# Performance work log

Measured on AMD Instinct MI355X. Metric: run time of the kernel, lower is better.

The kernel has to match this reference:

```python
import jax, jax.numpy as jnp
import numpy as np

B, S, D = 4, 2048, 1024
N_HEAD = 16
D_HEAD = D // N_HEAD
WINDOW = 1024
D_FF = 4 * D
EPS = 1e-5
NEG = -1e10


def _layernorm(x, g, b):
    mu = jnp.mean(x, axis=-1, keepdims=True)
    var = jnp.mean(jnp.square(x - mu), axis=-1, keepdims=True)
    return (x - mu) * jax.lax.rsqrt(var + EPS) * g + b


def setup_inputs() -> dict:
    key = jax.random.key(0)
    ks = jax.random.split(key, 12)
    s = 1.0 / np.sqrt(D)
    x = jax.random.normal(ks[0], (B, S, D), dtype=jnp.float32)
    key_pad_mask = jax.random.bernoulli(ks[1], 0.1, (B, S))
    return {
        "x": x,
        "key_pad_mask": key_pad_mask,
        "ln1_g": jnp.ones((D,), jnp.float32),
        "ln1_b": jnp.zeros((D,), jnp.float32),
        "wq": jax.random.normal(ks[2], (D, D), jnp.float32) * s,
        "bq": jnp.zeros((D,), jnp.float32),
        "wkv": jax.random.normal(ks[3], (D, 2 * D), jnp.float32) * s,
        "bkv": jnp.zeros((2 * D,), jnp.float32),
        "ln2_g": jnp.ones((D,), jnp.float32),
        "ln2_b": jnp.zeros((D,), jnp.float32),
        "w1": jax.random.normal(ks[4], (D, D_FF), jnp.float32) * s,
        "b1": jnp.zeros((D_FF,), jnp.float32),
        "w2": jax.random.normal(ks[5], (D_FF, D), jnp.float32) * (1.0 / np.sqrt(D_FF)),
        "b2": jnp.zeros((D,), jnp.float32),
    }


def reference(x, key_pad_mask, ln1_g, ln1_b, wq, bq, wkv, bkv, ln2_g, ln2_b, w1, b1, w2, b2):
    ln1x = _layernorm(x, ln1_g, ln1_b)
    # queries over full sequence: [B, S, nh, dh]
    q = (ln1x @ wq + bq).reshape(B, S, N_HEAD, D_HEAD)
    # keys/values from the last WINDOW tokens: [B, W, 2*nh, dh]
    kv = (ln1x[:, -WINDOW:, :] @ wkv + bkv).reshape(B, WINDOW, 2 * N_HEAD, D_HEAD)
    k, v = kv[..., :N_HEAD, :], kv[..., N_HEAD:, :]
    # NOTE: original scales by sqrt(embed_dim), not sqrt(head_dim)
    scores = jnp.einsum('bqhd,bkhd->bhqk', q, k) / np.sqrt(D)
    causal = jnp.triu(jnp.ones((S, WINDOW), dtype=bool), k=1)  # faithful to original
    pad = key_pad_mask[:, None, None, -WINDOW:]
    scores = jnp.where(pad | causal[None, None], jnp.float32(NEG), scores)
    attn = jax.nn.softmax(scores, axis=-1)
    out = jnp.einsum('bhqk,bkhd->bqhd', attn, v).reshape(B, S, D)
    h = _layernorm(out, ln2_g, ln2_b)
    h = jax.nn.silu(h @ w1 + b1) @ w2 + b2
    return h + x
```

## Files before the change

kernel.cpp:

```cpp
#include <hip/hip_runtime.h>
#include <hip/hip_bf16.h>

#define BB 4
#define SS 2048
#define DD 1024
#define HH 16
#define DHH 64
#define WW 1024
#define DFF 4096
#define MM (BB*SS)
#define NEGV (-1e10f)
#define KSC 0.045084220027780106f

using f32x4 = __attribute__((ext_vector_type(4))) float;
using s16x8 = __attribute__((ext_vector_type(8))) short;
using s16x4 = __attribute__((ext_vector_type(4))) short;
using u64 = unsigned long long;

typedef const __attribute__((address_space(1))) void* gas_t;
typedef __attribute__((address_space(3))) void* las_t;

__device__ inline short f2b(float f) {
  __hip_bfloat16 h = __float2bfloat16(f);
  return __builtin_bit_cast(short, h);
}
__device__ inline float b2f(short u) {
  __hip_bfloat16 h = __builtin_bit_cast(__hip_bfloat16, u);
  return __bfloat162float(h);
}

__device__ inline void gload_lds16(const short* g, short* lds) {
  __builtin_amdgcn_global_load_lds((gas_t)g, (las_t)lds, 16, 0, 0);
}

__device__ inline f32x4 mfma16(s16x8 a, s16x8 b, f32x4 c) {
  return __builtin_amdgcn_mfma_f32_16x16x32_bf16(a, b, c, 0, 0, 0);
}

template<int IN_BF16>
__global__ __launch_bounds__(256) void ln_kernel(const void* __restrict__ inp,
                                                 const float* __restrict__ g,
                                                 const float* __restrict__ bta,
                                                 short* __restrict__ outp) {
  int row = blockIdx.x;
  int t = threadIdx.x;
  float v[4];
  if constexpr (IN_BF16) {
    s16x4 r4 = *((const s16x4*)((const short*)inp + (size_t)row*DD) + t);
    v[0]=b2f(r4[0]); v[1]=b2f(r4[1]); v[2]=b2f(r4[2]); v[3]=b2f(r4[3]);
  } else {
    f32x4 r4 = *((const f32x4*)((const float*)inp + (size_t)row*DD) + t);
    v[0]=r4[0]; v[1]=r4[1]; v[2]=r4[2]; v[3]=r4[3];
  }
  float s = v[0]+v[1]+v[2]+v[3];
  float sq = v[0]*v[0]+v[1]*v[1]+v[2]*v[2]+v[3]*v[3];
  for (int m=1;m<64;m<<=1){ s += __shfl_xor(s,m); sq += __shfl_xor(sq,m); }
  __shared__ float red[8];
  int wv = t>>6;
  if ((t&63)==0){ red[wv]=s; red[4+wv]=sq; }
  __syncthreads();
  s  = red[0]+red[1]+red[2]+red[3];
  sq = red[4]+red[5]+red[6]+red[7];
  float mean = s*(1.f/DD);
  float rstd = rsqrtf(sq*(1.f/DD) - mean*mean + 1e-5f);
  int col = t*4;
  s16x4 o;
  #pragma unroll
  for (int j=0;j<4;++j) o[j] = f2b((v[j]-mean)*rstd*g[col+j]+bta[col+j]);
  *((s16x4*)(outp + (size_t)row*DD) + t) = o;
}

__global__ __launch_bounds__(256) void transpose_cast(const float* __restrict__ in,
                                                      short* __restrict__ out,
                                                      int K, int N) {
  __shared__ float tile[32][33];
  int n0 = blockIdx.x*32, k0 = blockIdx.y*32;
  int tx = threadIdx.x & 31, ty = threadIdx.x >> 5;
  #pragma unroll
  for (int j=0;j<4;++j) tile[ty+8*j][tx] = in[(size_t)(k0+ty+8*j)*N + n0+tx];
  __syncthreads();
  #pragma unroll
  for (int j=0;j<4;++j) out[(size_t)(n0+ty+8*j)*K + k0+tx] = f2b(tile[tx][ty+8*j]);
}

__global__ void pad_bitmask(const int* __restrict__ pad, u64* __restrict__ pm) {
  int idx = threadIdx.x;
  int b_ = idx>>4, col = idx&15;
  const int* pb = pad + b_*SS + (SS-WW);
  u64 m = 0;
  for (int c=0;c<16;++c)
    for (int nf=0;nf<4;++nf)
      if (pb[c*64+nf*16+col]) m |= (1ull << (c*4+nf));
  pm[idx] = m;
}

template<int EPI>
__global__ __launch_bounds__(512) void gemm256(const short* __restrict__ A,
                                               const short* __restrict__ Bt,
                                               const float* __restrict__ bias,
                                               void* __restrict__ out1,
                                               int N, int K, int lgx) {
  __shared__ short lds[32768];
  int tid = threadIdx.x, l = tid&63, wid = tid>>6;
  int wm = wid>>2, wn = wid&3;
  int q8 = gridDim.x >> 3;
  int wg = (blockIdx.x & 7)*q8 + (blockIdx.x >> 3);
  int bx = wg & ((1<<lgx)-1), by = wg >> lgx;
  const short* Ablk = A + (size_t)by*256*K;
  const short* Bblk = Bt + (size_t)bx*256*K;
  int rA = l & 15;
  int slot_s = ((l>>4) ^ ((rA>>1)&3))*8;
  int aBase = (wm*128 + rA)*32 + slot_s;
  int bBase = (wn*64  + rA)*32 + slot_s + 8192;
  int qs = (tid&3) ^ ((tid>>3)&3);
  const short* srcA = Ablk + (size_t)(tid>>2)*K + qs*8;
  const short* srcB = Bblk + (size_t)(tid>>2)*K + qs*8;
  int dst0 = (tid & ~63)*8;
  int nt = K >> 5;
  f32x4 acc[8][4];
  #pragma unroll
  for (int i=0;i<8;++i)
    #pragma unroll
    for (int j=0;j<4;++j)
      #pragma unroll
      for (int r=0;r<4;++r) acc[i][j][r]=0.f;

  auto stage = [&](int isB, int b, int t) {
    const short* s = isB ? srcB : srcA;
    short* d = &lds[b*16384 + isB*8192 + dst0];
    gload_lds16(s + t*32,                 d);
    gload_lds16(s + (size_t)128*K + t*32, d + 4096);
  };
  s16x8 af[4], bf[4];
  auto readA = [&](int b, int mg) {
    #pragma unroll
    for (int j=0;j<4;++j) af[j] = *(const s16x8*)&lds[b*16384 + aBase + (mg*4+j)*512];
  };
  auto readB = [&](int b) {
    #pragma unroll
    for (int j=0;j<4;++j) bf[j] = *(const s16x8*)&lds[b*16384 + bBase + j*512];
  };
  auto mfmas = [&](int mg) {
    __builtin_amdgcn_s_setprio(1);
    #pragma unroll
    for (int j=0;j<4;++j)
      #pragma unroll
      for (int nf=0;nf<4;++nf)
        acc[mg*4+j][nf] = mfma16(af[j], bf[nf], acc[mg*4+j][nf]);
    __builtin_amdgcn_s_setprio(0);
  };

  stage(0,0,0); stage(1,0,0); stage(1,1,1);
  asm volatile("s_waitcnt vmcnt(2)" ::: "memory");
  __builtin_amdgcn_s_barrier();

  for (int it = 0; it < (nt>>1); ++it) {
    int t0 = 2*it;
    int t2 = t0+2; if (t2 >= nt) t2 -= nt;
    int t3 = t0+3; if (t3 >= nt) t3 -= nt;
    readB(0); readA(0,0);
    stage(0,1,t0+1);
    __builtin_amdgcn_s_barrier();
    mfmas(0);
    __builtin_amdgcn_s_barrier();
    readA(0,1);
    stage(1,0,t2);
    __builtin_amdgcn_s_barrier();
    mfmas(1);
    asm volatile("s_waitcnt vmcnt(2)" ::: "memory");
    __builtin_amdgcn_s_barrier();
    readB(1); readA(1,0);
    stage(0,0,t2);
    __builtin_amdgcn_s_barrier();
    mfmas(0);
    __builtin_amdgcn_s_barrier();
    readA(1,1);
    stage(1,1,t3);
    __builtin_amdgcn_s_barrier();
    mfmas(1);
    asm volatile("s_waitcnt vmcnt(2)" ::: "memory");
    __builtin_amdgcn_s_barrier();
  }
  asm volatile("s_waitcnt vmcnt(0)" ::: "memory");

  #pragma unroll
  for (int mf=0;mf<8;++mf) {
    #pragma unroll
    for (int nf=0;nf<4;++nf) {
      #pragma unroll
      for (int r=0;r<4;++r) {
        int row = by*256 + wm*128 + mf*16 + ((l>>4)<<2) + r;
        int col = bx*256 + wn*64 + nf*16 + rA;
        float v = acc[mf][nf][r] + bias[col];
        if constexpr (EPI==2) {
          float sv = v / (1.f + __expf(-v));
          ((short*)out1)[(size_t)row*N + col] = f2b(sv);
        } else {
          ((short*)out1)[(size_t)row*N + col] = f2b(v);
        }
      }
    }
  }
}

template<int EPI>
__global__ __launch_bounds__(512) void gemm256x128(const short* __restrict__ A,
                                                   const short* __restrict__ Bt,
                                                   const float* __restrict__ bias,
                                                   void* __restrict__ out1,
                                                   void* __restrict__ out2,
                                                   const float* __restrict__ resid,
                                                   int N, int K, int lgx) {
  __shared__ short lds[24576];
  int tid = threadIdx.x, l = tid&63, wid = tid>>6;
  int wm = wid>>1, wn = wid&1;
  int q8 = gridDim.x >> 3;
  int wg = (blockIdx.x & 7)*q8 + (blockIdx.x >> 3);
  int bx = wg & ((1<<lgx)-1), by = wg >> lgx;
  const short* Ablk;
  if constexpr (EPI==1) {
    int b_ = (by*256)>>10, w0 = (by*256)&1023;
    Ablk = A + ((size_t)b_*SS + (SS-WW) + w0)*DD;
  } else {
    Ablk = A + (size_t)by*256*K;
  }
  const short* Bblk = Bt + (size_t)bx*128*K;
  int rA = l & 15;
  int slot_s = ((l>>4) ^ ((rA>>1)&3))*8;
  int aBase = (wm*64 + rA)*32 + slot_s;
  int bBase = 8192 + (wn*64 + rA)*32 + slot_s;
  int qs = (tid&3) ^ ((tid>>3)&3);
  const short* srcA = Ablk + (size_t)(tid>>2)*K + qs*8;
  const short* srcB = Bblk + (size_t)(tid>>2)*K + qs*8;
  int dst0 = (tid & ~63)*8;
  int nt = K >> 5;
  f32x4 acc[4][4];
  #pragma unroll
  for (int i=0;i<4;++i)
    #pragma unroll
    for (int j=0;j<4;++j)
      #pragma unroll
      for (int r=0;r<4;++r) acc[i][j][r]=0.f;

  auto stageA = [&](int b, int t) {
    short* d = &lds[b*12288 + dst0];
    gload_lds16(srcA + t*32,                 d);
    gload_lds16(srcA + (size_t)128*K + t*32, d + 4096);
  };
  auto stageB = [&](int b, int t) {
    gload_lds16(srcB + t*32, &lds[b*12288 + 8192 + dst0]);
  };
  s16x8 af[2], bf[4];
  auto readA = [&](int b, int mg) {
    #pragma unroll
    for (int j=0;j<2;++j) af[j] = *(const s16x8*)&lds[b*12288 + aBase + (mg*2+j)*512];
  };
  auto readB = [&](int b) {
    #pragma unroll
    for (int j=0;j<4;++j) bf[j] = *(const s16x8*)&lds[b*12288 + bBase + j*512];
  };
  auto mfmas = [&](int mg) {
    __builtin_amdgcn_s_setprio(1);
    #pragma unroll
    for (int j=0;j<2;++j)
      #pragma unroll
      for (int nf=0;nf<4;++nf)
        acc[mg*2+j][nf] = mfma16(af[j], bf[nf], acc[mg*2+j][nf]);
    __builtin_amdgcn_s_setprio(0);
  };

  stageA(0,0); stageB(0,0); stageB(1,1);
  asm volatile("s_waitcnt vmcnt(1)" ::: "memory");
  __builtin_amdgcn_s_barrier();

  for (int it = 0; it < (nt>>1); ++it) {
    int t0 = 2*it;
    int t2 = t0+2; if (t2 >= nt) t2 -= nt;
    int t3 = t0+3; if (t3 >= nt) t3 -= nt;
    readB(0); readA(0,0);
    stageA(1,t0+1);
    __builtin_amdgcn_s_barrier();
    mfmas(0);
    __builtin_amdgcn_s_barrier();
    readA(0,1);
    stageB(0,t2);
    __builtin_amdgcn_s_barrier();
    mfmas(1);
    asm volatile("s_waitcnt vmcnt(1)" ::: "memory");
    __builtin_amdgcn_s_barrier();
    readB(1); readA(1,0);
    stageA(0,t2);
    __builtin_amdgcn_s_barrier();
    mfmas(0);
    __builtin_amdgcn_s_barrier();
    readA(1,1);
    stageB(1,t3);
    __builtin_amdgcn_s_barrier();
    mfmas(1);
    asm volatile("s_waitcnt vmcnt(1)" ::: "memory");
    __builtin_amdgcn_s_barrier();
  }
  asm volatile("s_waitcnt vmcnt(0)" ::: "memory");

  #pragma unroll
  for (int mf=0;mf<4;++mf) {
    #pragma unroll
    for (int nf=0;nf<4;++nf) {
      #pragma unroll
      for (int r=0;r<4;++r) {
        int row = by*256 + wm*64 + mf*16 + ((l>>4)<<2) + r;
        int col = bx*128 + wn*64 + nf*16 + rA;
        float v = acc[mf][nf][r] + bias[col];
        if constexpr (EPI==0) {
          ((short*)out1)[(size_t)row*N + col] = f2b(v);
        } else if constexpr (EPI==1) {
          int b_ = row>>10, w_ = row&1023;
          if (col < DD) {
            int h = col>>6, dh = col&63;
            ((short*)out1)[(((size_t)(b_*HH+h))*WW + w_)*DHH + dh] = f2b(v*KSC);
          } else {
            int cc = col - DD;
            int h = cc>>6, dh = cc&63;
            ((short*)out2)[(((size_t)(b_*HH+h))*DHH + dh)*WW + w_] = f2b(v);
          }
        } else {
          ((float*)out1)[(size_t)row*N + col] = v + resid[(size_t)row*N + col];
        }
      }
    }
  }
}

struct KF { s16x8 v[4][2]; };

__global__ __launch_bounds__(64,2) void attn_kernel(const short* __restrict__ q,
    const short* __restrict__ kpan, const short* __restrict__ vtpan,
    const u64* __restrict__ pmarr, short* __restrict__ outp) {
  __shared__ short P[32*72];
  int l = threadIdx.x;
  int id = blockIdx.x;
  int xcd = id & 7, slot = id >> 3;
  int bh = xcd + 8*(slot >> 6);
  int u  = 63 - (slot & 63);
  int bb = bh >> 4, h = bh & 15;
  int r0 = u*32;
  const short* kbase = kpan + (size_t)bh*WW*DHH;
  const short* vbase = vtpan + (size_t)bh*DHH*WW;
  u64 pmask = pmarr[bb*16 + (l&15)];
  const s16x8 ones8 = { 0x3F80,0x3F80,0x3F80,0x3F80,0x3F80,0x3F80,0x3F80,0x3F80 };

  s16x8 aq[2][2];
  #pragma unroll
  for (int g=0;g<2;++g)
    #pragma unroll
    for (int kf=0;kf<2;++kf)
      aq[g][kf] = *(const s16x8*)(q + ((size_t)bb*SS + r0 + g*16 + (l&15))*DD
                                    + h*DHH + (l>>4)*8 + kf*32);
  f32x4 oacc[2][4];
  float mrun[2][4], lrun[2][4], scale[2][4];
  #pragma unroll
  for (int g=0;g<2;++g)
    #pragma unroll
    for (int i=0;i<4;++i) {
      #pragma unroll
      for (int r=0;r<4;++r) oacc[g][i][r]=0.f;
      mrun[g][i]=-INFINITY; lrun[g][i]=0.f;
    }
  int dchunk = u>>1;
  int nch = dchunk+1 < 16 ? dchunk+1 : 16;

  auto loadK = [&](int c, KF& d) {
    const short* kc = kbase + (size_t)c*64*DHH;
    #pragma unroll
    for (int nf=0;nf<4;++nf) {
      const short* p = kc + (size_t)(nf*16+(l&15))*DHH + ((l>>4)*8);
      d.v[nf][0] = *(const s16x8*)p;
      d.v[nf][1] = *(const s16x8*)(p+32);
    }
  };

  auto body = [&](int c, KF& kf) {
    f32x4 sc[2][4];
    #pragma unroll
    for (int g=0;g<2;++g)
      #pragma unroll
      for (int nf=0;nf<4;++nf)
        #pragma unroll
        for (int r=0;r<4;++r) sc[g][nf][r]=0.f;
    __builtin_amdgcn_s_setprio(1);
    #pragma unroll
    for (int nf=0;nf<4;++nf)
      #pragma unroll
      for (int g=0;g<2;++g) {
        sc[g][nf] = mfma16(aq[g][0], kf.v[nf][0], sc[g][nf]);
        sc[g][nf] = mfma16(aq[g][1], kf.v[nf][1], sc[g][nf]);
      }
    __builtin_amdgcn_s_setprio(0);
    unsigned nib = (unsigned)(pmask >> (c*4)) & 15u;
    float pm[2][4];
    #pragma unroll
    for (int g=0;g<2;++g)
      #pragma unroll
      for (int r=0;r<4;++r) pm[g][r] = -INFINITY;
    if (c >= dchunk) {
      #pragma unroll
      for (int nf=0;nf<4;++nf) {
        int j = c*64 + nf*16 + (l&15);
        int padj = (int)((nib>>nf)&1u);
        #pragma unroll
        for (int g=0;g<2;++g)
          #pragma unroll
          for (int r=0;r<4;++r) {
            int sq_ = r0 + g*16 + ((l>>4)<<2) + r;
            float xv = (padj || (j > sq_)) ? NEGV : sc[g][nf][r];
            sc[g][nf][r] = xv;
            pm[g][r] = fmaxf(pm[g][r], xv);
          }
      }
    } else {
      #pragma unroll
      for (int nf=0;nf<4;++nf) {
        int padj = (int)((nib>>nf)&1u);
        #pragma unroll
        for (int g=0;g<2;++g)
          #pragma unroll
          for (int r=0;r<4;++r) {
            float xv = padj ? NEGV : sc[g][nf][r];
            sc[g][nf][r] = xv;
            pm[g][r] = fmaxf(pm[g][r], xv);
          }
      }
    }
    s16x8 vf0[4], vf1[4];
    #pragma unroll
    for (int nf=0;nf<4;++nf)
      vf0[nf] = *(const s16x8*)(vbase + (size_t)(nf*16+(l&15))*WW
                                + c*64 + ((l>>4)*8));
    int need = 0;
    #pragma unroll
    for (int g=0;g<2;++g)
      #pragma unroll
      for (int r=0;r<4;++r) need |= (pm[g][r] > mrun[g][r] + 12.f) ? 1 : 0;
    #pragma unroll
    for (int g=0;g<2;++g)
      #pragma unroll
      for (int r=0;r<4;++r) scale[g][r] = 1.f;
    if (__any(need)) {
      #pragma unroll
      for (int m=1;m<16;m<<=1)
        #pragma unroll
        for (int g=0;g<2;++g)
          #pragma unroll
          for (int r=0;r<4;++r) pm[g][r] = fmaxf(pm[g][r], __shfl_xor(pm[g][r], m));
      #pragma unroll
      for (int g=0;g<2;++g)
        #pragma unroll
        for (int r=0;r<4;++r) {
          float mn = fmaxf(mrun[g][r], pm[g][r]);
          scale[g][r] = exp2f(mrun[g][r]-mn);
          mrun[g][r] = mn;
        }
      #pragma unroll
      for (int g=0;g<2;++g)
        #pragma unroll
        for (int nf=0;nf<4;++nf)
          #pragma unroll
          for (int r=0;r<4;++r) oacc[g][nf][r] *= scale[g][r];
    }
    #pragma unroll
    for (int nf=0;nf<4;++nf)
      #pragma unroll
      for (int g=0;g<2;++g)
        #pragma unroll
        for (int r=0;r<4;++r)
          sc[g][nf][r] = exp2f(sc[g][nf][r]-mrun[g][r]);
    #pragma unroll
    for (int nf=0;nf<4;++nf)
      vf1[nf] = *(const s16x8*)(vbase + (size_t)(nf*16+(l&15))*WW
                                + c*64 + 32 + ((l>>4)*8));
    #pragma unroll
    for (int g=0;g<2;++g)
      #pragma unroll
      for (int nf=0;nf<4;++nf)
        #pragma unroll
        for (int r=0;r<4;++r)
          P[(g*16+((l>>4)<<2)+r)*72 + nf*16 + (l&15)] = f2b(sc[g][nf][r]);
    f32x4 ls2[2];
    #pragma unroll
    for (int g=0;g<2;++g)
      #pragma unroll
      for (int r=0;r<4;++r) ls2[g][r]=0.f;
    __builtin_amdgcn_s_setprio(1);
    #pragma unroll
    for (int ks=0;ks<2;++ks) {
      s16x8 ap[2];
      #pragma unroll
      for (int g=0;g<2;++g) {
        ap[g] = *(const s16x8*)&P[(g*16+(l&15))*72 + ks*32 + ((l>>4)*8)];
        ls2[g] = mfma16(ap[g], ones8, ls2[g]);
      }
      #pragma unroll
      for (int nf=0;nf<4;++nf) {
        s16x8 bv = ks ? vf1[nf] : vf0[nf];
        #pragma unroll
        for (int g=0;g<2;++g)
          oacc[g][nf] = mfma16(ap[g], bv, oacc[g][nf]);
      }
    }
    __builtin_amdgcn_s_setprio(0);
    #pragma unroll
    for (int g=0;g<2;++g)
      #pragma unroll
      for (int r=0;r<4;++r) lrun[g][r] = lrun[g][r]*scale[g][r] + ls2[g][r];
  };

  KF ka, kb;
  loadK(0, ka);
  int cend = nch, c = 0, ext = 0;
  while (true) {
    if (c == cend) {
      if (ext) break;
      ext = 1;
      int dead = 0;
      #pragma unroll
      for (int g=0;g<2;++g)
        #pragma unroll
        for (int r=0;r<4;++r) dead |= (mrun[g][r] < -5e9f) ? 1 : 0;
      if (!__any(dead)) break;
      cend = 16;
      if (c >= 16) break;
    }
    if (c+1 < 16) loadK(c+1, kb);
    body(c, ka);
    ka = kb;
    ++c;
  }

  #pragma unroll
  for (int g=0;g<2;++g)
    #pragma unroll
    for (int nf=0;nf<4;++nf)
      #pragma unroll
      for (int r=0;r<4;++r) {
        int srow = r0 + g*16 + ((l>>4)<<2) + r;
        float o = oacc[g][nf][r] / lrun[g][r];
        outp[((size_t)bb*SS + srow)*DD + h*DHH + nf*16 + (l&15)] = f2b(o);
      }
}

extern "C" void kernel_launch(void* const* d_in, const int* in_sizes, int n_in,
                              void* d_out, int out_size, void* d_ws, size_t ws_size,
                              hipStream_t stream) {
  const float* x    = (const float*)d_in[0];
  const int*   pad  = (const int*)d_in[1];
  const float* ln1g = (const float*)d_in[2];
  const float* ln1b = (const float*)d_in[3];
  const float* wq   = (const float*)d_in[4];
  const float* bq   = (const float*)d_in[5];
  const float* wkv  = (const float*)d_in[6];
  const float* bkv  = (const float*)d_in[7];
  const float* ln2g = (const float*)d_in[8];
  const float* ln2b = (const float*)d_in[9];
  const float* w1   = (const float*)d_in[10];
  const float* b1   = (const float*)d_in[11];
  const float* w2   = (const float*)d_in[12];
  const float* b2   = (const float*)d_in[13];

  char* ws = (char*)d_ws;
  const size_t MB = 1024*1024;
  short* ln1x = (short*)(ws + 0);
  short* qb   = (short*)(ws + 16*MB);
  short* kpan = (short*)(ws + 32*MB);
  short* vtp  = (short*)(ws + 40*MB);
  u64*   pmar = (u64*)  (ws + 48*MB);
  short* h1   = (short*)(ws + 0);
  short* outb = (short*)(ws + 64*MB);
  short* hb   = (short*)(ws + 80*MB);
  short* wqT  = (short*)(ws + 96*MB);
  short* wkvT = (short*)(ws + 98*MB);
  short* w1T  = (short*)(ws + 102*MB);
  short* w2T  = (short*)(ws + 110*MB);

  pad_bitmask<<<1,64,0,stream>>>(pad, pmar);
  transpose_cast<<<dim3(32,32),  256,0,stream>>>(wq,  wqT,  1024, 1024);
  transpose_cast<<<dim3(64,32),  256,0,stream>>>(wkv, wkvT, 1024, 2048);
  transpose_cast<<<dim3(128,32), 256,0,stream>>>(w1,  w1T,  1024, 4096);
  transpose_cast<<<dim3(32,128), 256,0,stream>>>(w2,  w2T,  4096, 1024);
  ln_kernel<0><<<MM,256,0,stream>>>(x, ln1g, ln1b, ln1x);
  gemm256x128<0><<<256,512,0,stream>>>(ln1x, wqT,  bq,  qb,   nullptr, nullptr, 1024, 1024, 3);
  gemm256x128<1><<<256,512,0,stream>>>(ln1x, wkvT, bkv, kpan, vtp,     nullptr, 2048, 1024, 4);
  attn_kernel<<<4096,64,0,stream>>>(qb, kpan, vtp, pmar, outb);
  ln_kernel<1><<<MM,256,0,stream>>>(outb, ln2g, ln2b, hb);
  gemm256<2><<<512,512,0,stream>>>(hb, w1T, b1, h1, 4096, 1024, 4);
  gemm256x128<3><<<256,512,0,stream>>>(h1, w2T, b2, d_out, nullptr, x, 1024, 4096, 3);
}
```

Baseline: 366.1 us.

## Software-pipeline attention QK and softmax/PV, pack four waves per block

The attention kernel now launches 256-thread blocks in which four independent waves each handle one 32-row query tile, each with its own LDS P buffer. The chunk loop is split into a QK MFMA stage and a mask/softmax/PV stage, arranged so the QK scores of the next chunk are computed before the previous chunk's softmax. This lets matrix work overlap the exp and shuffle work. It also skips the per-element masking when a chunk has no padded keys and is not on the diagonal. The cost is a second score register set (sA/sB), which raises register pressure and may hurt occupancy.

```diff
diff --git a/kernel.cpp b/kernel.cpp
--- a/kernel.cpp
+++ b/kernel.cpp
@@ -333,21 +333,22 @@
 
 struct KF { s16x8 v[4][2]; };
 
-__global__ __launch_bounds__(64,2) void attn_kernel(const short* __restrict__ q,
+__global__ __launch_bounds__(256,2) void attn_kernel(const short* __restrict__ q,
     const short* __restrict__ kpan, const short* __restrict__ vtpan,
     const u64* __restrict__ pmarr, short* __restrict__ outp) {
-  __shared__ short P[32*72];
-  int l = threadIdx.x;
-  int id = blockIdx.x;
-  int xcd = id & 7, slot = id >> 3;
-  int bh = xcd + 8*(slot >> 6);
-  int u  = 63 - (slot & 63);
+  __shared__ short P[4][32*72];
+  int tid = threadIdx.x, l = tid&63, wv = tid>>6;
+  int pb = blockIdx.x;
+  int xcd = pb & 7, s = pb >> 3;
+  int bh = xcd + 8*(s>>4);
+  int u  = 63 - ((s&15)*4 + wv);
   int bb = bh >> 4, h = bh & 15;
   int r0 = u*32;
   const short* kbase = kpan + (size_t)bh*WW*DHH;
   const short* vbase = vtpan + (size_t)bh*DHH*WW;
   u64 pmask = pmarr[bb*16 + (l&15)];
   const s16x8 ones8 = { 0x3F80,0x3F80,0x3F80,0x3F80,0x3F80,0x3F80,0x3F80,0x3F80 };
+  short* Pw = &P[wv][0];
 
   s16x8 aq[2][2];
   #pragma unroll
@@ -357,7 +358,7 @@
       aq[g][kf] = *(const s16x8*)(q + ((size_t)bb*SS + r0 + g*16 + (l&15))*DD
                                     + h*DHH + (l>>4)*8 + kf*32);
   f32x4 oacc[2][4];
-  float mrun[2][4], lrun[2][4], scale[2][4];
+  float mrun[2][4], lrun[2][4];
   #pragma unroll
   for (int g=0;g<2;++g)
     #pragma unroll
@@ -367,7 +368,7 @@
       mrun[g][i]=-INFINITY; lrun[g][i]=0.f;
     }
   int dchunk = u>>1;
-  int nch = dchunk+1 < 16 ? dchunk+1 : 16;
+  int cend = dchunk+1 < 16 ? dchunk+1 : 16;
 
   auto loadK = [&](int c, KF& d) {
     const short* kc = kbase + (size_t)c*64*DHH;
@@ -379,8 +380,7 @@
     }
   };
 
-  auto body = [&](int c, KF& kf) {
-    f32x4 sc[2][4];
+  auto QK = [&](KF& kf, f32x4 (&sc)[2][4]) {
     #pragma unroll
     for (int g=0;g<2;++g)
       #pragma unroll
@@ -396,46 +396,60 @@
         sc[g][nf] = mfma16(aq[g][1], kf.v[nf][1], sc[g][nf]);
       }
     __builtin_amdgcn_s_setprio(0);
+  };
+
+  auto SMPV = [&](int c, f32x4 (&sc)[2][4]) {
     unsigned nib = (unsigned)(pmask >> (c*4)) & 15u;
+    int diag = (c >= dchunk);
     float pm[2][4];
     #pragma unroll
     for (int g=0;g<2;++g)
       #pragma unroll
       for (int r=0;r<4;++r) pm[g][r] = -INFINITY;
-    if (c >= dchunk) {
-      #pragma unroll
-      for (int nf=0;nf<4;++nf) {
-        int j = c*64 + nf*16 + (l&15);
-        int padj = (int)((nib>>nf)&1u);
+    if (diag || __any(nib != 0u)) {
+      if (diag) {
+        #pragma unroll
+        for (int nf=0;nf<4;++nf) {
+          int j = c*64 + nf*16 + (l&15);
+          int padj = (int)((nib>>nf)&1u);
+          #pragma unroll
+          for (int g=0;g<2;++g)
+            #pragma unroll
+            for (int r=0;r<4;++r) {
+              int sq_ = r0 + g*16 + ((l>>4)<<2) + r;
+              float xv = (padj || (j > sq_)) ? NEGV : sc[g][nf][r];
+              sc[g][nf][r] = xv;
+              pm[g][r] = fmaxf(pm[g][r], xv);
+            }
+        }
+      } else {
+        #pragma unroll
+        for (int nf=0;nf<4;++nf) {
+          int padj = (int)((nib>>nf)&1u);
+          #pragma unroll
+          for (int g=0;g<2;++g)
+            #pragma unroll
+            for (int r=0;r<4;++r) {
+              float xv = padj ? NEGV : sc[g][nf][r];
+              sc[g][nf][r] = xv;
+              pm[g][r] = fmaxf(pm[g][r], xv);
+            }
+        }
+      }
+    } else {
+      #pragma unroll
+      for (int nf=0;nf<4;++nf)
         #pragma unroll
         for (int g=0;g<2;++g)
           #pragma unroll
-          for (int r=0;r<4;++r) {
-            int sq_ = r0 + g*16 + ((l>>4)<<2) + r;
-            float xv = (padj || (j > sq_)) ? NEGV : sc[g][nf][r];
-            sc[g][nf][r] = xv;
-            pm[g][r] = fmaxf(pm[g][r], xv);
-          }
-      }
-    } else {
-      #pragma unroll
-      for (int nf=0;nf<4;++nf) {
-        int padj = (int)((nib>>nf)&1u);
-        #pragma unroll
-        for (int g=0;g<2;++g)
-          #pragma unroll
-          for (int r=0;r<4;++r) {
-            float xv = padj ? NEGV : sc[g][nf][r];
-            sc[g][nf][r] = xv;
-            pm[g][r] = fmaxf(pm[g][r], xv);
-          }
-      }
+          for (int r=0;r<4;++r) pm[g][r] = fmaxf(pm[g][r], sc[g][nf][r]);
     }
     s16x8 vf0[4], vf1[4];
     #pragma unroll
     for (int nf=0;nf<4;++nf)
       vf0[nf] = *(const s16x8*)(vbase + (size_t)(nf*16+(l&15))*WW
                                 + c*64 + ((l>>4)*8));
+    float scale[2][4];
     int need = 0;
     #pragma unroll
     for (int g=0;g<2;++g)
@@ -484,7 +498,7 @@
       for (int nf=0;nf<4;++nf)
         #pragma unroll
         for (int r=0;r<4;++r)
-          P[(g*16+((l>>4)<<2)+r)*72 + nf*16 + (l&15)] = f2b(sc[g][nf][r]);
+          Pw[(g*16+((l>>4)<<2)+r)*72 + nf*16 + (l&15)] = f2b(sc[g][nf][r]);
     f32x4 ls2[2];
     #pragma unroll
     for (int g=0;g<2;++g)
@@ -496,7 +510,7 @@
       s16x8 ap[2];
       #pragma unroll
       for (int g=0;g<2;++g) {
-        ap[g] = *(const s16x8*)&P[(g*16+(l&15))*72 + ks*32 + ((l>>4)*8)];
+        ap[g] = *(const s16x8*)&Pw[(g*16+(l&15))*72 + ks*32 + ((l>>4)*8)];
         ls2[g] = mfma16(ap[g], ones8, ls2[g]);
       }
       #pragma unroll
@@ -515,25 +529,38 @@
   };
 
   KF ka, kb;
+  f32x4 sA[2][4], sB[2][4];
   loadK(0, ka);
-  int cend = nch, c = 0, ext = 0;
-  while (true) {
-    if (c == cend) {
-      if (ext) break;
-      ext = 1;
-      int dead = 0;
-      #pragma unroll
-      for (int g=0;g<2;++g)
-        #pragma unroll
-        for (int r=0;r<4;++r) dead |= (mrun[g][r] < -5e9f) ? 1 : 0;
-      if (!__any(dead)) break;
-      cend = 16;
-      if (c >= 16) break;
-    }
-    if (c+1 < 16) loadK(c+1, kb);
-    body(c, ka);
-    ka = kb;
-    ++c;
+  QK(ka, sA);
+  loadK(1, kb);
+  int c = 1;
+  for (; c+1 < cend; c += 2) {
+    QK(kb, sB);
+    if (c+1 < 16) loadK(c+1, ka);
+    SMPV(c-1, sA);
+    QK(ka, sA);
+    if (c+2 < 16) loadK(c+2, kb);
+    SMPV(c, sB);
+  }
+  if (c < cend) {
+    QK(kb, sB);
+    SMPV(c-1, sA);
+    SMPV(c, sB);
+  } else {
+    SMPV(c-1, sA);
+  }
+
+  int dead = 0;
+  #pragma unroll
+  for (int g=0;g<2;++g)
+    #pragma unroll
+    for (int r=0;r<4;++r) dead |= (mrun[g][r] < -5e9f) ? 1 : 0;
+  if (__any(dead)) {
+    for (int e=cend; e<16; ++e) {
+      loadK(e, ka);
+      QK(ka, sA);
+      SMPV(e, sA);
+    }
   }
 
   #pragma unroll
@@ -589,7 +616,7 @@
   ln_kernel<0><<<MM,256,0,stream>>>(x, ln1g, ln1b, ln1x);
   gemm256x128<0><<<256,512,0,stream>>>(ln1x, wqT,  bq,  qb,   nullptr, nullptr, 1024, 1024, 3);
   gemm256x128<1><<<256,512,0,stream>>>(ln1x, wkvT, bkv, kpan, vtp,     nullptr, 2048, 1024, 4);
-  attn_kernel<<<4096,64,0,stream>>>(qb, kpan, vtp, pmar, outb);
+  attn_kernel<<<1024,256,0,stream>>>(qb, kpan, vtp, pmar, outb);
   ln_kernel<1><<<MM,256,0,stream>>>(outb, ln2g, ln2b, hb);
   gemm256<2><<<512,512,0,stream>>>(hb, w1T, b1, h1, 4096, 1024, 4);
   gemm256x128<3><<<256,512,0,stream>>>(h1, w2T, b2, d_out, nullptr, x, 1024, 4096, 3);
```

New measurement: 388.1 us. 1.06x slower.

## Switch GEMM LDS pipeline to triple-buffered ring with two tiles in flight

Applied to the files above, without the earlier changes.

Replaces the GEMM's two-buffer, half-stage staggered prefetch schedule with a three-region LDS ring. Each iteration computes on the current region while loading the tile two steps ahead, waiting with vmcnt(4) so two tiles stay in flight. This aims to hide global-load latency better. In exchange LDS use per block rises from 64KB to 96KB, and the ring indices are now runtime-variable, which can add address arithmetic and limit occupancy.

```diff
diff --git a/kernel.cpp b/kernel.cpp
--- a/kernel.cpp
+++ b/kernel.cpp
@@ -100,7 +100,7 @@
                                                const float* __restrict__ bias,
                                                void* __restrict__ out1,
                                                int N, int K, int lgx) {
-  __shared__ short lds[32768];
+  __shared__ short lds[49152];
   int tid = threadIdx.x, l = tid&63, wid = tid>>6;
   int wm = wid>>2, wn = wid&3;
   int q8 = gridDim.x >> 3;
@@ -125,20 +125,20 @@
       #pragma unroll
       for (int r=0;r<4;++r) acc[i][j][r]=0.f;
 
-  auto stage = [&](int isB, int b, int t) {
+  auto stage = [&](int isB, int rgn, int t) {
     const short* s = isB ? srcB : srcA;
-    short* d = &lds[b*16384 + isB*8192 + dst0];
+    short* d = &lds[rgn*16384 + isB*8192 + dst0];
     gload_lds16(s + t*32,                 d);
     gload_lds16(s + (size_t)128*K + t*32, d + 4096);
   };
   s16x8 af[4], bf[4];
-  auto readA = [&](int b, int mg) {
-    #pragma unroll
-    for (int j=0;j<4;++j) af[j] = *(const s16x8*)&lds[b*16384 + aBase + (mg*4+j)*512];
-  };
-  auto readB = [&](int b) {
-    #pragma unroll
-    for (int j=0;j<4;++j) bf[j] = *(const s16x8*)&lds[b*16384 + bBase + j*512];
+  auto readA = [&](int rgn, int mg) {
+    #pragma unroll
+    for (int j=0;j<4;++j) af[j] = *(const s16x8*)&lds[rgn*16384 + aBase + (mg*4+j)*512];
+  };
+  auto readB = [&](int rgn) {
+    #pragma unroll
+    for (int j=0;j<4;++j) bf[j] = *(const s16x8*)&lds[rgn*16384 + bBase + j*512];
   };
   auto mfmas = [&](int mg) {
     __builtin_amdgcn_s_setprio(1);
@@ -150,36 +150,27 @@
     __builtin_amdgcn_s_setprio(0);
   };
 
-  stage(0,0,0); stage(1,0,0); stage(1,1,1);
-  asm volatile("s_waitcnt vmcnt(2)" ::: "memory");
+  stage(0,0,0); stage(1,0,0);
+  stage(0,1,1); stage(1,1,1);
+  asm volatile("s_waitcnt vmcnt(4)" ::: "memory");
   __builtin_amdgcn_s_barrier();
 
-  for (int it = 0; it < (nt>>1); ++it) {
-    int t0 = 2*it;
-    int t2 = t0+2; if (t2 >= nt) t2 -= nt;
-    int t3 = t0+3; if (t3 >= nt) t3 -= nt;
-    readB(0); readA(0,0);
-    stage(0,1,t0+1);
+  int cur = 0, s2 = 2;
+  for (int t = 0; t < nt; ++t) {
+    int ts = t+2; if (ts >= nt) ts -= nt;
+    readB(cur); readA(cur,0);
+    stage(0, s2, ts);
     __builtin_amdgcn_s_barrier();
     mfmas(0);
     __builtin_amdgcn_s_barrier();
-    readA(0,1);
-    stage(1,0,t2);
+    readA(cur,1);
+    stage(1, s2, ts);
     __builtin_amdgcn_s_barrier();
     mfmas(1);
-    asm volatile("s_waitcnt vmcnt(2)" ::: "memory");
-    __builtin_amdgcn_s_barrier();
-    readB(1); readA(1,0);
-    stage(0,0,t2);
-    __builtin_amdgcn_s_barrier();
-    mfmas(0);
-    __builtin_amdgcn_s_barrier();
-    readA(1,1);
-    stage(1,1,t3);
-    __builtin_amdgcn_s_barrier();
-    mfmas(1);
-    asm volatile("s_waitcnt vmcnt(2)" ::: "memory");
-    __builtin_amdgcn_s_barrier();
+    asm volatile("s_waitcnt vmcnt(4)" ::: "memory");
+    __builtin_amdgcn_s_barrier();
+    cur = (cur+1==3) ? 0 : cur+1;
+    s2  = (s2+1==3)  ? 0 : s2+1;
   }
   asm volatile("s_waitcnt vmcnt(0)" ::: "memory");
 
```

After: 372.2 us. About the same (+1.7%).

## Software-pipeline attention: overlap QK of next chunk with PV of previous

Applied to the files above, without the earlier changes.

Splits the attention loop body into QK, softmax and PV stages. The QK MFMAs for chunk c are now interleaved with the PV MFMAs for chunk c-1, and the P tile in LDS is double-buffered so the two chunks do not collide. The aim is to hide the dependency latency between softmax and PV, and the V load latency. The cost is more live registers, plus a restructured fallback path that handles rows still fully masked after the causal range.

```diff
diff --git a/kernel.cpp b/kernel.cpp
--- a/kernel.cpp
+++ b/kernel.cpp
@@ -336,7 +336,7 @@
 __global__ __launch_bounds__(64,2) void attn_kernel(const short* __restrict__ q,
     const short* __restrict__ kpan, const short* __restrict__ vtpan,
     const u64* __restrict__ pmarr, short* __restrict__ outp) {
-  __shared__ short P[32*72];
+  __shared__ short P[2][32*72];
   int l = threadIdx.x;
   int id = blockIdx.x;
   int xcd = id & 7, slot = id >> 3;
@@ -357,17 +357,17 @@
       aq[g][kf] = *(const s16x8*)(q + ((size_t)bb*SS + r0 + g*16 + (l&15))*DD
                                     + h*DHH + (l>>4)*8 + kf*32);
   f32x4 oacc[2][4];
-  float mrun[2][4], lrun[2][4], scale[2][4];
+  float mrun[2][4], lrun[2][4], scp[2][4];
   #pragma unroll
   for (int g=0;g<2;++g)
     #pragma unroll
     for (int i=0;i<4;++i) {
       #pragma unroll
       for (int r=0;r<4;++r) oacc[g][i][r]=0.f;
-      mrun[g][i]=-INFINITY; lrun[g][i]=0.f;
+      mrun[g][i]=-INFINITY; lrun[g][i]=0.f; scp[g][i]=1.f;
     }
   int dchunk = u>>1;
-  int nch = dchunk+1 < 16 ? dchunk+1 : 16;
+  int cend = dchunk+1 < 16 ? dchunk+1 : 16;
 
   auto loadK = [&](int c, KF& d) {
     const short* kc = kbase + (size_t)c*64*DHH;
@@ -379,8 +379,9 @@
     }
   };
 
-  auto body = [&](int c, KF& kf) {
-    f32x4 sc[2][4];
+  f32x4 sc[2][4];
+
+  auto QK = [&](KF& kf) {
     #pragma unroll
     for (int g=0;g<2;++g)
       #pragma unroll
@@ -396,6 +397,51 @@
         sc[g][nf] = mfma16(aq[g][1], kf.v[nf][1], sc[g][nf]);
       }
     __builtin_amdgcn_s_setprio(0);
+  };
+
+  auto loadV = [&](int c, s16x8 (&vf0)[4], s16x8 (&vf1)[4]) {
+    #pragma unroll
+    for (int nf=0;nf<4;++nf)
+      vf0[nf] = *(const s16x8*)(vbase + (size_t)(nf*16+(l&15))*WW
+                                + c*64 + ((l>>4)*8));
+    #pragma unroll
+    for (int nf=0;nf<4;++nf)
+      vf1[nf] = *(const s16x8*)(vbase + (size_t)(nf*16+(l&15))*WW
+                                + c*64 + 32 + ((l>>4)*8));
+  };
+
+  auto PV = [&](int c, s16x8 (&vf0)[4], s16x8 (&vf1)[4]) {
+    f32x4 ls2[2];
+    #pragma unroll
+    for (int g=0;g<2;++g)
+      #pragma unroll
+      for (int r=0;r<4;++r) ls2[g][r]=0.f;
+    const short* Pb = &P[c&1][0];
+    __builtin_amdgcn_s_setprio(1);
+    #pragma unroll
+    for (int ks=0;ks<2;++ks) {
+      s16x8 ap[2];
+      #pragma unroll
+      for (int g=0;g<2;++g) {
+        ap[g] = *(const s16x8*)&Pb[(g*16+(l&15))*72 + ks*32 + ((l>>4)*8)];
+        ls2[g] = mfma16(ap[g], ones8, ls2[g]);
+      }
+      #pragma unroll
+      for (int nf=0;nf<4;++nf) {
+        s16x8 bv = ks ? vf1[nf] : vf0[nf];
+        #pragma unroll
+        for (int g=0;g<2;++g)
+          oacc[g][nf] = mfma16(ap[g], bv, oacc[g][nf]);
+      }
+    }
+    __builtin_amdgcn_s_setprio(0);
+    #pragma unroll
+    for (int g=0;g<2;++g)
+      #pragma unroll
+      for (int r=0;r<4;++r) lrun[g][r] = lrun[g][r]*scp[g][r] + ls2[g][r];
+  };
+
+  auto SM = [&](int c) {
     unsigned nib = (unsigned)(pmask >> (c*4)) & 15u;
     float pm[2][4];
     #pragma unroll
@@ -431,11 +477,6 @@
           }
       }
     }
-    s16x8 vf0[4], vf1[4];
-    #pragma unroll
-    for (int nf=0;nf<4;++nf)
-      vf0[nf] = *(const s16x8*)(vbase + (size_t)(nf*16+(l&15))*WW
-                                + c*64 + ((l>>4)*8));
     int need = 0;
     #pragma unroll
     for (int g=0;g<2;++g)
@@ -444,7 +485,7 @@
     #pragma unroll
     for (int g=0;g<2;++g)
       #pragma unroll
-      for (int r=0;r<4;++r) scale[g][r] = 1.f;
+      for (int r=0;r<4;++r) scp[g][r] = 1.f;
     if (__any(need)) {
       #pragma unroll
       for (int m=1;m<16;m<<=1)
@@ -457,7 +498,7 @@
         #pragma unroll
         for (int r=0;r<4;++r) {
           float mn = fmaxf(mrun[g][r], pm[g][r]);
-          scale[g][r] = exp2f(mrun[g][r]-mn);
+          scp[g][r] = exp2f(mrun[g][r]-mn);
           mrun[g][r] = mn;
         }
       #pragma unroll
@@ -465,7 +506,7 @@
         #pragma unroll
         for (int nf=0;nf<4;++nf)
           #pragma unroll
-          for (int r=0;r<4;++r) oacc[g][nf][r] *= scale[g][r];
+          for (int r=0;r<4;++r) oacc[g][nf][r] *= scp[g][r];
     }
     #pragma unroll
     for (int nf=0;nf<4;++nf)
@@ -474,66 +515,49 @@
         #pragma unroll
         for (int r=0;r<4;++r)
           sc[g][nf][r] = exp2f(sc[g][nf][r]-mrun[g][r]);
-    #pragma unroll
-    for (int nf=0;nf<4;++nf)
-      vf1[nf] = *(const s16x8*)(vbase + (size_t)(nf*16+(l&15))*WW
-                                + c*64 + 32 + ((l>>4)*8));
+    short* Pb = &P[c&1][0];
     #pragma unroll
     for (int g=0;g<2;++g)
       #pragma unroll
       for (int nf=0;nf<4;++nf)
         #pragma unroll
         for (int r=0;r<4;++r)
-          P[(g*16+((l>>4)<<2)+r)*72 + nf*16 + (l&15)] = f2b(sc[g][nf][r]);
-    f32x4 ls2[2];
-    #pragma unroll
-    for (int g=0;g<2;++g)
-      #pragma unroll
-      for (int r=0;r<4;++r) ls2[g][r]=0.f;
-    __builtin_amdgcn_s_setprio(1);
-    #pragma unroll
-    for (int ks=0;ks<2;++ks) {
-      s16x8 ap[2];
-      #pragma unroll
-      for (int g=0;g<2;++g) {
-        ap[g] = *(const s16x8*)&P[(g*16+(l&15))*72 + ks*32 + ((l>>4)*8)];
-        ls2[g] = mfma16(ap[g], ones8, ls2[g]);
-      }
-      #pragma unroll
-      for (int nf=0;nf<4;++nf) {
-        s16x8 bv = ks ? vf1[nf] : vf0[nf];
-        #pragma unroll
-        for (int g=0;g<2;++g)
-          oacc[g][nf] = mfma16(ap[g], bv, oacc[g][nf]);
-      }
-    }
-    __builtin_amdgcn_s_setprio(0);
-    #pragma unroll
-    for (int g=0;g<2;++g)
-      #pragma unroll
-      for (int r=0;r<4;++r) lrun[g][r] = lrun[g][r]*scale[g][r] + ls2[g][r];
+          Pb[(g*16+((l>>4)<<2)+r)*72 + nf*16 + (l&15)] = f2b(sc[g][nf][r]);
   };
 
   KF ka, kb;
   loadK(0, ka);
-  int cend = nch, c = 0, ext = 0;
-  while (true) {
-    if (c == cend) {
-      if (ext) break;
-      ext = 1;
-      int dead = 0;
-      #pragma unroll
-      for (int g=0;g<2;++g)
-        #pragma unroll
-        for (int r=0;r<4;++r) dead |= (mrun[g][r] < -5e9f) ? 1 : 0;
-      if (!__any(dead)) break;
-      cend = 16;
-      if (c >= 16) break;
-    }
+  int c = 0;
+  while (c < cend) {
     if (c+1 < 16) loadK(c+1, kb);
-    body(c, ka);
+    s16x8 vf0[4], vf1[4];
+    if (c > 0) loadV(c-1, vf0, vf1);
+    QK(ka);
+    if (c > 0) PV(c-1, vf0, vf1);
+    SM(c);
     ka = kb;
     ++c;
+  }
+  {
+    s16x8 vf0[4], vf1[4];
+    loadV(cend-1, vf0, vf1);
+    PV(cend-1, vf0, vf1);
+  }
+
+  int dead = 0;
+  #pragma unroll
+  for (int g=0;g<2;++g)
+    #pragma unroll
+    for (int r=0;r<4;++r) dead |= (mrun[g][r] < -5e9f) ? 1 : 0;
+  if (__any(dead)) {
+    for (int e=cend; e<16; ++e) {
+      loadK(e, ka);
+      s16x8 vf0[4], vf1[4];
+      loadV(e, vf0, vf1);
+      QK(ka);
+      SM(e);
+      PV(e, vf0, vf1);
+    }
   }
 
   #pragma unroll
```

Result: no change. 367.2 us, median of 2 (+0.3%).
